# Performance work log

Hardware: AMD Instinct MI355X
Metric: run time of the kernel (lower is better)

## Reference

```python
import jax, jax.numpy as jnp
import numpy as np

# Dims
B_, L_, IN_ = 16, 8192, 57
DM, DS, HD, EXP, NL, OUT = 64, 32, 32, 2, 2, 6
DI = EXP * DM            # 128 inner dim
NH = DI // HD            # 4 heads
DPROJ = 2 * DI + 2 * DS + NH  # z, x, B, C, dt


def setup_inputs() -> dict:
    key = jax.random.key(0)
    ks = jax.random.split(key, 8)
    def rn(k, shape, scale=0.02):
        return jax.random.normal(k, shape, dtype=jnp.float32) * scale
    return {
        "x": jax.random.normal(ks[0], (B_, L_, IN_), dtype=jnp.float32),
        "W_in": rn(ks[1], (IN_, DM)),
        "b_in": jnp.zeros((DM,), jnp.float32),
        "in_proj_W": rn(ks[2], (NL, DM, DPROJ)),
        "in_proj_b": jnp.zeros((NL, DPROJ), jnp.float32),
        "A_log": jnp.log(jnp.broadcast_to(jnp.arange(1, NH + 1, dtype=jnp.float32), (NL, NH))),
        "D": jnp.ones((NL, NH), jnp.float32),
        "dt_bias": rn(ks[3], (NL, NH), 0.1),
        "out_proj_W": rn(ks[4], (NL, DI, DM)),
        "out_proj_b": jnp.zeros((NL, DM), jnp.float32),
        "cls_W": rn(ks[5], (DM, OUT)),
        "cls_b": jnp.zeros((OUT,), jnp.float32),
    }


def _mamba_layer(x, W, b, A_log, D, dt_bias, Wo, bo):
    """SISO Mamba3-style selective scan block. x: [B, L, DM]."""
    Bsz, L, _ = x.shape
    zxbcdt = x @ W + b                               # [B, L, DPROJ]
    z, xin, Bm, Cm, dt = jnp.split(
        zxbcdt, [DI, 2 * DI, 2 * DI + DS, 2 * DI + 2 * DS], axis=-1)
    dt = jax.nn.softplus(dt + dt_bias)               # [B, L, NH]
    A = -jnp.exp(A_log)                              # [NH], per-head scalar (SISO)
    xin = jax.nn.silu(xin).reshape(Bsz, L, NH, HD)   # [B, L, NH, HD]
    Bm = jax.nn.silu(Bm)                             # [B, L, DS]
    Cm = jax.nn.silu(Cm)                             # [B, L, DS]
    decay = jnp.exp(dt * A)                          # [B, L, NH]

    def step(h, inp):
        # h: [B, NH, HD, DS]
        xt, bt, ct, dtt, dect = inp
        h = dect[:, :, None, None] * h + (dtt[:, :, None] * xt)[..., None] * bt[:, None, None, :]
        yt = jnp.einsum('bhpn,bn->bhp', h, ct)       # [B, NH, HD]
        return h, yt

    h0 = jnp.zeros((Bsz, NH, HD, DS), x.dtype)
    xs = (jnp.moveaxis(xin, 1, 0), jnp.moveaxis(Bm, 1, 0), jnp.moveaxis(Cm, 1, 0),
          jnp.moveaxis(dt, 1, 0), jnp.moveaxis(decay, 1, 0))
    _, ys = jax.lax.scan(step, h0, xs)               # [L, B, NH, HD]
    y = jnp.moveaxis(ys, 0, 1) + D[None, None, :, None] * xin
    y = y.reshape(Bsz, L, DI) * jax.nn.silu(z)       # gated output
    return y @ Wo + bo                               # [B, L, DM]


def reference(x, W_in, b_in, in_proj_W, in_proj_b, A_log, D, dt_bias,
              out_proj_W, out_proj_b, cls_W, cls_b):
    h = x @ W_in + b_in                              # linear_in
    for l in range(NL):                              # residual Mamba stack
        h = h + _mamba_layer(h, in_proj_W[l], in_proj_b[l], A_log[l], D[l],
                             dt_bias[l], out_proj_W[l], out_proj_b[l])
    pooled = h.mean(axis=1)                          # AdaptiveAvgPool1d(1)
    return pooled @ cls_W + cls_b                    # classifier [B, OUT]
```

## Files before the change

### kernel.cpp

```cpp
#include <hip/hip_runtime.h>

#define BSZ   16
#define LSEQ  8192
#define DMDL  64
#define DSD   32
#define HDD   32
#define NHD   4
#define DIN   128
#define NLAY  2
#define NOUTC 6
#define DPRJ  324
#define QC    64
#define NCH   128
#define NT21  21

typedef __attribute__((ext_vector_type(8))) short bf16x8;
typedef __attribute__((ext_vector_type(4))) float f32x4;

__device__ float          g_h0[BSZ*LSEQ*DMDL];
__device__ unsigned short g_xy[BSZ*LSEQ*DIN];
__device__ unsigned short g_Ca[BSZ*LSEQ*DSD];
__device__ float          g_pc[BSZ*LSEQ*NHD];
__device__ float          g_cS[BSZ*NCH*NHD*HDD*DSD];
__device__ unsigned short g_Hb[BSZ*NCH*NHD*HDD*DSD];
__device__ float          g_cL[BSZ*NCH*NHD];
__device__ float          g_ppc[BSZ*NCH*DMDL];
__device__ unsigned short g_wf[NLAY*NT21*2*64*8];
__device__ unsigned short g_wo[NLAY*4*4*64*8];

__device__ __forceinline__ float silu_f(float v){ return v / (1.0f + __expf(-v)); }
__device__ __forceinline__ float softplus_f(float v){ return (v > 15.0f) ? v : __logf(1.0f + __expf(v)); }
__device__ __forceinline__ unsigned short f2bf(float f){
  union { float f; unsigned u; } v; v.f = f;
  unsigned r = v.u + 0x7FFFu + ((v.u >> 16) & 1u);
  return (unsigned short)(r >> 16);
}
__device__ __forceinline__ float bf2f(unsigned short h){
  union { unsigned u; float f; } v; v.u = ((unsigned)h) << 16;
  return v.f;
}

#define LSTR 132
__global__ __launch_bounds__(256) void k_linin(
    const float* __restrict__ x, const float* __restrict__ W,
    const float* __restrict__ bias)
{
  __shared__ float xt[57*LSTR];
  __shared__ float wl[57*64];
  const int tid = threadIdx.x;
  const long tb = (long)blockIdx.x * 128;
  for (int i = tid; i < 912; i += 256)
    *(float4*)&wl[i*4] = *(const float4*)&W[i*4];
  for (int i = tid; i < 1824; i += 256){
    float4 v = *(const float4*)&x[tb*57 + (long)i*4];
    const int e = i*4;
    int t0 = e / 57;
    int k0 = e - t0*57;
    float vv[4] = {v.x, v.y, v.z, v.w};
    #pragma unroll
    for (int j = 0; j < 4; ++j){
      int t = t0, k = k0 + j;
      if (k >= 57){ t += 1; k -= 57; }
      xt[k*LSTR + t] = vv[j];
    }
  }
  __syncthreads();
  const int d0 = (tid & 7) * 8;
  const int t0 = (tid >> 3) * 4;
  float acc[4][8];
  #pragma unroll
  for (int i = 0; i < 4; ++i)
    #pragma unroll
    for (int j = 0; j < 8; ++j) acc[i][j] = 0.f;
  #pragma unroll 4
  for (int k = 0; k < 57; ++k){
    float4 xv4 = *(const float4*)&xt[k*LSTR + t0];
    float4 w0  = *(const float4*)&wl[k*64 + d0];
    float4 w1  = *(const float4*)&wl[k*64 + d0 + 4];
    float xv[4] = {xv4.x, xv4.y, xv4.z, xv4.w};
    float wv[8] = {w0.x, w0.y, w0.z, w0.w, w1.x, w1.y, w1.z, w1.w};
    #pragma unroll
    for (int i = 0; i < 4; ++i)
      #pragma unroll
      for (int j = 0; j < 8; ++j) acc[i][j] += xv[i] * wv[j];
  }
  float4 bb0 = *(const float4*)&bias[d0];
  float4 bb1 = *(const float4*)&bias[d0 + 4];
  #pragma unroll
  for (int i = 0; i < 4; ++i){
    float4 o0, o1;
    o0.x = acc[i][0] + bb0.x; o0.y = acc[i][1] + bb0.y;
    o0.z = acc[i][2] + bb0.z; o0.w = acc[i][3] + bb0.w;
    o1.x = acc[i][4] + bb1.x; o1.y = acc[i][5] + bb1.y;
    o1.z = acc[i][6] + bb1.z; o1.w = acc[i][7] + bb1.w;
    *(float4*)&g_h0[(tb + t0 + i)*64 + d0]     = o0;
    *(float4*)&g_h0[(tb + t0 + i)*64 + d0 + 4] = o1;
  }
}

__global__ __launch_bounds__(128) void k_wprep(const float* __restrict__ W)
{
  const int nt = blockIdx.x;
  const int l  = blockIdx.y;
  const int ks = threadIdx.x >> 6, lane = threadIdx.x & 63;
  const float* Wl = W + (long)l*64*DPRJ;
  const int n  = nt*16 + (lane & 15);
  const int k0 = ks*32 + (lane >> 4)*8;
  unsigned short v[8];
  #pragma unroll
  for (int j = 0; j < 8; ++j)
    v[j] = (n < DPRJ) ? f2bf(Wl[(k0 + j)*DPRJ + n]) : (unsigned short)0;
  unsigned short* d = &g_wf[((((long)l*NT21 + nt)*2 + ks)*64 + lane)*8];
  *(ushort4*)&d[0] = make_ushort4(v[0], v[1], v[2], v[3]);
  *(ushort4*)&d[4] = make_ushort4(v[4], v[5], v[6], v[7]);
}

__global__ __launch_bounds__(64) void k_wprep2(const float* __restrict__ Wo)
{
  const int nt = blockIdx.x >> 2, ks = blockIdx.x & 3, l = blockIdx.y;
  const int lane = threadIdx.x;
  const int n  = nt*16 + (lane & 15);
  const int k0 = ks*32 + (lane >> 4)*8;
  const float* Wl = Wo + (long)l*128*64;
  unsigned short* d = &g_wo[((((long)l*4 + nt)*4 + ks)*64 + lane)*8];
  unsigned short v[8];
  #pragma unroll
  for (int j = 0; j < 8; ++j) v[j] = f2bf(Wl[(k0 + j)*64 + n]);
  *(ushort4*)&d[0] = make_ushort4(v[0], v[1], v[2], v[3]);
  *(ushort4*)&d[4] = make_ushort4(v[4], v[5], v[6], v[7]);
}

#define SB 40
#define ST 72
__device__ __forceinline__ int xsw(int p, int s){
  return p*ST + (((((s) >> 3) + ((p) >> 2)) & 7) << 3) + ((s) & 7);
}
__device__ __forceinline__ int xsw8(int p, int blk){
  return p*ST + (((((blk)) + ((p) >> 2)) & 7) << 3);
}
__global__ __launch_bounds__(256) void k_ps(
    const float* __restrict__ ipb, const float* __restrict__ dtb,
    const float* __restrict__ A_log, const float* __restrict__ Dp, int l)
{
  __shared__ __align__(16) unsigned short Afr[4*2*64*8];
  __shared__ __align__(16) unsigned short Bb[64*SB];
  __shared__ __align__(16) unsigned short Cb[64*SB];
  __shared__ __align__(16) unsigned short Bbt[32*ST];
  __shared__ __align__(16) unsigned short Xt[32*ST];
  __shared__ __align__(16) unsigned short Mb[64*ST];
  __shared__ float Sl[4*64];
  __shared__ float dts[4*64];
  __shared__ float wls[4*64];
  __shared__ float dtl[64*4];
  const int tid = threadIdx.x;
  const int cI = blockIdx.x, b = blockIdx.y;
  const long tb = (long)b*LSEQ + (long)cI*QC;
  for (int i = tid; i < 512; i += 256){
    const int t = i >> 3, k8 = i & 7;
    float4 f0 = *(const float4*)&g_h0[(tb + t)*64 + k8*8];
    float4 f1 = *(const float4*)&g_h0[(tb + t)*64 + k8*8 + 4];
    const int mt = t >> 4, ks = k8 >> 2, q = k8 & 3, ln = (t & 15) + 16*q;
    unsigned short* d = &Afr[(((mt*2 + ks)*64) + ln)*8];
    *(ushort4*)&d[0] = make_ushort4(f2bf(f0.x), f2bf(f0.y), f2bf(f0.z), f2bf(f0.w));
    *(ushort4*)&d[4] = make_ushort4(f2bf(f1.x), f2bf(f1.y), f2bf(f1.z), f2bf(f1.w));
  }
  __syncthreads();
  const int w = tid >> 6, lane = tid & 63;
  const int colq = lane & 15, rowq = lane >> 4;
  const float* bl = ipb + (long)l*DPRJ;
  const unsigned short* wf = &g_wf[(long)l*NT21*2*64*8];
  const bf16x8 a0 = *(const bf16x8*)&Afr[((w*2 + 0)*64 + lane)*8];
  const bf16x8 a1 = *(const bf16x8*)&Afr[((w*2 + 1)*64 + lane)*8];
  #pragma unroll
  for (int nti = 0; nti < 4; ++nti){
    const int nt = 16 + nti;
    bf16x8 b0 = *(const bf16x8*)&wf[((nt*2 + 0)*64 + lane)*8];
    bf16x8 b1 = *(const bf16x8*)&wf[((nt*2 + 1)*64 + lane)*8];
    const float bia = bl[nt*16 + colq];
    f32x4 acc = {0.f, 0.f, 0.f, 0.f};
    acc = __builtin_amdgcn_mfma_f32_16x16x32_bf16(a0, b0, acc, 0, 0, 0);
    acc = __builtin_amdgcn_mfma_f32_16x16x32_bf16(a1, b1, acc, 0, 0, 0);
    const int t4 = w*16 + rowq*4;
    if (nti < 2){
      const int n = nti*16 + colq;
      #pragma unroll
      for (int r = 0; r < 4; ++r){
        const unsigned short v = f2bf(silu_f(acc[r] + bia));
        Bb[(t4 + r)*SB + n] = v;
        Bbt[xsw(n, t4 + r)] = v;
      }
    } else {
      const int n = (nti - 2)*16 + colq;
      #pragma unroll
      for (int r = 0; r < 4; ++r)
        Cb[(t4 + r)*SB + n] = f2bf(silu_f(acc[r] + bia));
    }
  }
  {
    bf16x8 b0 = *(const bf16x8*)&wf[((20*2 + 0)*64 + lane)*8];
    bf16x8 b1 = *(const bf16x8*)&wf[((20*2 + 1)*64 + lane)*8];
    f32x4 acc = {0.f, 0.f, 0.f, 0.f};
    acc = __builtin_amdgcn_mfma_f32_16x16x32_bf16(a0, b0, acc, 0, 0, 0);
    acc = __builtin_amdgcn_mfma_f32_16x16x32_bf16(a1, b1, acc, 0, 0, 0);
    if (colq < 4){
      const float bia = bl[320 + colq] + dtb[l*4 + colq];
      const int t4 = w*16 + rowq*4;
      #pragma unroll
      for (int r = 0; r < 4; ++r)
        dtl[(t4 + r)*4 + colq] = softplus_f(acc[r] + bia);
    }
  }
  __syncthreads();
  {
    const int h = w, t = lane;
    const float Ah = -__expf(A_log[l*4 + h]);
    const float v = dtl[t*4 + h];
    float x = v * Ah;
    #pragma unroll
    for (int d = 1; d < 64; d <<= 1){
      float y = __shfl_up(x, d);
      if (t >= d) x += y;
    }
    Sl[h*64 + t] = x;
    dts[h*64 + t] = v;
    const float send = __shfl(x, 63);
    wls[h*64 + t] = __expf(send - x) * v;
    if (t == 63) g_cL[((long)b*NCH + cI)*4 + h] = x;
    g_pc[(tb + t)*4 + h] = __expf(x);
  }
  {
    const int t = tid >> 2, c0 = (tid & 3) * 8;
    *(uint4*)&g_Ca[(tb + t)*32 + c0] = *(const uint4*)&Cb[t*SB + c0];
  }
  float Greg[3][4];
  int Gmt[3], Gst[3];
  #pragma unroll
  for (int rep = 0; rep < 3; ++rep){
    const int k = w + rep*4;
    if (k < 10){
      const int mt = (k >= 6) ? 3 : ((k >= 3) ? 2 : ((k >= 1) ? 1 : 0));
      const int st = k - mt*(mt+1)/2;
      Gmt[rep] = mt; Gst[rep] = st;
      bf16x8 af = *(const bf16x8*)&Cb[(mt*16 + colq)*SB + rowq*8];
      bf16x8 bf = *(const bf16x8*)&Bb[(st*16 + colq)*SB + rowq*8];
      f32x4 acc = {0.f, 0.f, 0.f, 0.f};
      acc = __builtin_amdgcn_mfma_f32_16x16x32_bf16(af, bf, acc, 0, 0, 0);
      #pragma unroll
      for (int r = 0; r < 4; ++r) Greg[rep][r] = acc[r];
    } else { Gmt[rep] = -1; Gst[rep] = 0; }
  }
  #pragma unroll
  for (int rep = 0; rep < 2; ++rep){
    const int k = w + rep*4;
    if (k < 6){
      const int mt = (k < 3) ? 0 : ((k < 5) ? 1 : 2);
      const int st = (k < 3) ? (k + 1) : ((k < 5) ? (k - 1) : 3);
      #pragma unroll
      for (int r = 0; r < 4; ++r){
        const int t = mt*16 + rowq*4 + r, s = st*16 + colq;
        Mb[xsw(t, s)] = 0;
      }
    }
  }
  __syncthreads();
  for (int h = 0; h < NHD; ++h){
    #pragma unroll
    for (int half = 0; half < 2; ++half){
      const int nt = 8 + 2*h + half;
      bf16x8 b0 = *(const bf16x8*)&wf[((nt*2 + 0)*64 + lane)*8];
      bf16x8 b1 = *(const bf16x8*)&wf[((nt*2 + 1)*64 + lane)*8];
      const float bia = bl[nt*16 + colq];
      f32x4 acc = {0.f, 0.f, 0.f, 0.f};
      acc = __builtin_amdgcn_mfma_f32_16x16x32_bf16(a0, b0, acc, 0, 0, 0);
      acc = __builtin_amdgcn_mfma_f32_16x16x32_bf16(a1, b1, acc, 0, 0, 0);
      const int p = half*16 + colq;
      const int t4 = w*16 + rowq*4;
      #pragma unroll
      for (int r = 0; r < 4; ++r)
        Xt[xsw(p, t4 + r)] = f2bf(silu_f(acc[r] + bia));
    }
    #pragma unroll
    for (int rep = 0; rep < 3; ++rep){
      if (Gmt[rep] >= 0){
        const int mt = Gmt[rep], st = Gst[rep];
        const int s = st*16 + colq;
        const float sls = Sl[h*64 + s];
        const float dv = dts[h*64 + s];
        #pragma unroll
        for (int r = 0; r < 4; ++r){
          const int t = mt*16 + rowq*4 + r;
          const float m = (s <= t) ? __expf(Sl[h*64 + t] - sls) * dv * Greg[rep][r] : 0.f;
          Mb[xsw(t, s)] = f2bf(m);
        }
      }
    }
    __syncthreads();
    const float Dh = Dp[l*4 + h];
    bf16x8 ma0 = *(const bf16x8*)&Mb[xsw8(w*16 + colq, rowq)];
    bf16x8 ma1 = *(const bf16x8*)&Mb[xsw8(w*16 + colq, rowq + 4)];
    bf16x8 xb0, xb1;
    #pragma unroll
    for (int nt = 0; nt < 2; ++nt){
      bf16x8 b0 = *(const bf16x8*)&Xt[xsw8(nt*16 + colq, rowq)];
      bf16x8 b1 = *(const bf16x8*)&Xt[xsw8(nt*16 + colq, rowq + 4)];
      if (nt == (w & 1)){ xb0 = b0; xb1 = b1; }
      f32x4 acc = {0.f, 0.f, 0.f, 0.f};
      acc = __builtin_amdgcn_mfma_f32_16x16x32_bf16(ma0, b0, acc, 0, 0, 0);
      acc = __builtin_amdgcn_mfma_f32_16x16x32_bf16(ma1, b1, acc, 0, 0, 0);
      const int p = nt*16 + colq;
      #pragma unroll
      for (int r = 0; r < 4; ++r){
        const int t = w*16 + rowq*4 + r;
        const float xv = bf2f(Xt[xsw(p, t)]);
        g_xy[(tb + t)*128 + h*32 + p] = f2bf(acc[r] + Dh*xv);
      }
    }
    {
      union { bf16x8 v; unsigned short u[8]; } sx0, sx1, sa0, sa1;
      sx0.v = xb0; sx1.v = xb1;
      #pragma unroll
      for (int j = 0; j < 8; ++j){
        sa0.u[j] = f2bf(bf2f(sx0.u[j]) * wls[h*64 + rowq*8 + j]);
        sa1.u[j] = f2bf(bf2f(sx1.u[j]) * wls[h*64 + 32 + rowq*8 + j]);
      }
      const int mt = w & 1, nt2 = w >> 1;
      bf16x8 bb0 = *(const bf16x8*)&Bbt[xsw8(nt2*16 + colq, rowq)];
      bf16x8 bb1 = *(const bf16x8*)&Bbt[xsw8(nt2*16 + colq, rowq + 4)];
      f32x4 acc = {0.f, 0.f, 0.f, 0.f};
      acc = __builtin_amdgcn_mfma_f32_16x16x32_bf16(sa0.v, bb0, acc, 0, 0, 0);
      acc = __builtin_amdgcn_mfma_f32_16x16x32_bf16(sa1.v, bb1, acc, 0, 0, 0);
      const long base = (((long)b*NCH + cI)*NHD + h)*(HDD*DSD);
      const int n = nt2*16 + colq;
      #pragma unroll
      for (int r = 0; r < 4; ++r){
        const int p = mt*16 + rowq*4 + r;
        g_cS[base + p*32 + n] = acc[r];
      }
    }
    __syncthreads();
  }
}

__global__ __launch_bounds__(128) void k_s2()
{
  const int h = blockIdx.x >> 3, seg = blockIdx.x & 7, b = blockIdx.y;
  const int idx = seg*128 + threadIdx.x;
  float H = 0.f;
  for (int c = 0; c < NCH; ++c){
    const long o = (((long)b*NCH + c)*NHD + h)*1024 + idx;
    const float cs = g_cS[o];
    const float lg = g_cL[((long)b*NCH + c)*4 + h];
    g_Hb[o] = f2bf(H);
    H = __expf(lg) * H + cs;
  }
}

__global__ __launch_bounds__(256) void k_s3(
    const float* __restrict__ ipb, const float* __restrict__ bo, int l, int finalLayer)
{
  __shared__ __align__(16) unsigned short Hb[128*40];
  __shared__ __align__(16) unsigned short Cb[64*40];
  __shared__ __align__(16) unsigned short gl[64*136];
  __shared__ float pcl[4*64];
  __shared__ float csum[4*64];
  const int tid = threadIdx.x;
  const int cI = blockIdx.x, b = blockIdx.y;
  const long tb = (long)b*LSEQ + (long)cI*QC;
  const long hbase = (((long)b*NCH + cI)*NHD)*(long)(HDD*DSD);
  for (int i = tid; i < 512; i += 256){
    const int hp = i >> 2, n0 = (i & 3) * 8;
    *(uint4*)&Hb[hp*40 + n0] = *(const uint4*)&g_Hb[hbase + hp*32 + n0];
  }
  for (int i = tid; i < 512; i += 256){
    const int t = i >> 3, n0 = (i & 7) * 4;
    *(ushort4*)&Cb[t*40 + n0] = *(const ushort4*)&g_Ca[(tb + t)*32 + n0];
  }
  { int t = tid >> 2, h = tid & 3; pcl[h*64 + t] = g_pc[(tb + t)*4 + h]; }
  __syncthreads();
  const int w = tid >> 6, lane = tid & 63;
  const int colq = lane & 15, rowq = lane >> 4;
  const float* blz = ipb + (long)l*DPRJ;
  const unsigned short* wfz = &g_wf[(long)l*NT21*2*64*8];
  {
    const long tok0 = tb + w*16 + colq;
    bf16x8 h0a, h0b;
    {
      float4 f0 = *(const float4*)&g_h0[tok0*64 + rowq*8];
      float4 f1 = *(const float4*)&g_h0[tok0*64 + rowq*8 + 4];
      float4 f2 = *(const float4*)&g_h0[tok0*64 + 32 + rowq*8];
      float4 f3 = *(const float4*)&g_h0[tok0*64 + 32 + rowq*8 + 4];
      union { bf16x8 v; unsigned short u[8]; } ca, cb2;
      ca.u[0]=f2bf(f0.x); ca.u[1]=f2bf(f0.y); ca.u[2]=f2bf(f0.z); ca.u[3]=f2bf(f0.w);
      ca.u[4]=f2bf(f1.x); ca.u[5]=f2bf(f1.y); ca.u[6]=f2bf(f1.z); ca.u[7]=f2bf(f1.w);
      cb2.u[0]=f2bf(f2.x); cb2.u[1]=f2bf(f2.y); cb2.u[2]=f2bf(f2.z); cb2.u[3]=f2bf(f2.w);
      cb2.u[4]=f2bf(f3.x); cb2.u[5]=f2bf(f3.y); cb2.u[6]=f2bf(f3.z); cb2.u[7]=f2bf(f3.w);
      h0a = ca.v; h0b = cb2.v;
    }
    bf16x8 a = *(const bf16x8*)&Cb[(w*16 + colq)*40 + rowq*8];
    #pragma unroll
    for (int nt = 0; nt < 8; ++nt){
      bf16x8 bfr = *(const bf16x8*)&Hb[(nt*16 + colq)*40 + rowq*8];
      f32x4 acc = {0.f, 0.f, 0.f, 0.f};
      acc = __builtin_amdgcn_mfma_f32_16x16x32_bf16(a, bfr, acc, 0, 0, 0);
      bf16x8 bz0 = *(const bf16x8*)&wfz[((nt*2 + 0)*64 + lane)*8];
      bf16x8 bz1 = *(const bf16x8*)&wfz[((nt*2 + 1)*64 + lane)*8];
      f32x4 zac = {0.f, 0.f, 0.f, 0.f};
      zac = __builtin_amdgcn_mfma_f32_16x16x32_bf16(h0a, bz0, zac, 0, 0, 0);
      zac = __builtin_amdgcn_mfma_f32_16x16x32_bf16(h0b, bz1, zac, 0, 0, 0);
      const int hp = nt*16 + colq;
      const int h = hp >> 5;
      const float zb = blz[hp];
      #pragma unroll
      for (int r = 0; r < 4; ++r){
        const int t = w*16 + rowq*4 + r;
        const long tok = tb + t;
        const float v = pcl[h*64 + t] * acc[r] + bf2f(g_xy[tok*128 + hp]);
        gl[t*136 + hp] = f2bf(v * silu_f(zac[r] + zb));
      }
    }
  }
  __syncthreads();
  const unsigned short* wo = &g_wo[(long)l*4*4*512];
  #pragma unroll
  for (int nt2 = 0; nt2 < 4; ++nt2){
    f32x4 acc = {0.f, 0.f, 0.f, 0.f};
    #pragma unroll
    for (int ks = 0; ks < 4; ++ks){
      bf16x8 a = *(const bf16x8*)&gl[(w*16 + colq)*136 + ks*32 + rowq*8];
      bf16x8 bfr = *(const bf16x8*)&wo[(nt2*4 + ks)*512 + lane*8];
      acc = __builtin_amdgcn_mfma_f32_16x16x32_bf16(a, bfr, acc, 0, 0, 0);
    }
    const int dm = nt2*16 + colq;
    const float bb = bo[l*64 + dm];
    float part = 0.f;
    #pragma unroll
    for (int r = 0; r < 4; ++r){
      const int t = w*16 + rowq*4 + r;
      const long tok = tb + t;
      const float o = acc[r] + bb + g_h0[tok*64 + dm];
      g_h0[tok*64 + dm] = o;
      part += o;
    }
    if (finalLayer){
      part += __shfl_xor(part, 16);
      part += __shfl_xor(part, 32);
      if (rowq == 0) csum[w*64 + dm] = part;
    }
  }
  if (finalLayer){
    __syncthreads();
    if (tid < 64){
      g_ppc[((long)b*NCH + cI)*64 + tid] =
        csum[tid] + csum[64 + tid] + csum[128 + tid] + csum[192 + tid];
    }
  }
}

__global__ __launch_bounds__(64) void k_pool2(
    const float* __restrict__ cW, const float* __restrict__ cb,
    float* __restrict__ out)
{
  __shared__ float pl[64];
  const int b = blockIdx.x, tid = threadIdx.x;
  float s = 0.f;
  for (int c = 0; c < NCH; ++c) s += g_ppc[((long)b*NCH + c)*64 + tid];
  pl[tid] = s * (1.0f / 8192.0f);
  __syncthreads();
  if (tid < NOUTC){
    float acc = cb[tid];
    for (int dm = 0; dm < 64; ++dm) acc += pl[dm] * cW[dm*NOUTC + tid];
    out[b*NOUTC + tid] = acc;
  }
}

extern "C" void kernel_launch(void* const* d_in, const int* in_sizes, int n_in,
                              void* d_out, int out_size, void* d_ws, size_t ws_size,
                              hipStream_t stream)
{
  const float* x      = (const float*)d_in[0];
  const float* W_in   = (const float*)d_in[1];
  const float* b_in   = (const float*)d_in[2];
  const float* ipW    = (const float*)d_in[3];
  const float* ipb    = (const float*)d_in[4];
  const float* A_log  = (const float*)d_in[5];
  const float* Dp     = (const float*)d_in[6];
  const float* dtb    = (const float*)d_in[7];
  const float* opW    = (const float*)d_in[8];
  const float* opb    = (const float*)d_in[9];
  const float* clsW   = (const float*)d_in[10];
  const float* clsb   = (const float*)d_in[11];
  float* out = (float*)d_out;
  (void)d_ws; (void)ws_size;

  k_wprep<<<dim3(NT21, NLAY), 128, 0, stream>>>(ipW);
  k_wprep2<<<dim3(16, NLAY), 64, 0, stream>>>(opW);
  k_linin<<<1024, 256, 0, stream>>>(x, W_in, b_in);
  for (int l = 0; l < NLAY; ++l){
    k_ps<<<dim3(NCH, BSZ), 256, 0, stream>>>(ipb, dtb, A_log, Dp, l);
    k_s2<<<dim3(32, BSZ), 128, 0, stream>>>();
    k_s3<<<dim3(NCH, BSZ), 256, 0, stream>>>(ipb, opb, l, (l == NLAY-1) ? 1 : 0);
  }
  k_pool2<<<BSZ, 64, 0, stream>>>(clsW, clsb, out);
}
```

Before: 319.9 us.

## Use packed bf16 conversion, store chunk states in bf16, double-buffer per-head LDS

Swaps the manual float-to-bf16 rounding for the hardware packed convert instruction and widens the LDS stores. The chunk-state buffer g_cS moves from fp32 to bf16, halving its write and read traffic between k_ps and k_s2. The per-head Xt and Mb scratch buffers are double-buffered (Xt reuses the A-fragment buffer) so the trailing barrier in the head loop can be dropped. k_s2's chunk loop is also unrolled. The risk is lower precision in the inter-chunk state accumulation, plus possible hazards if the double-buffer reuse of the A-fragment region is unsafe.

```diff
diff --git a/kernel.cpp b/kernel.cpp
--- a/kernel.cpp
+++ b/kernel.cpp
@@ -21,7 +21,7 @@
 __device__ unsigned short g_xy[BSZ*LSEQ*DIN];
 __device__ unsigned short g_Ca[BSZ*LSEQ*DSD];
 __device__ float          g_pc[BSZ*LSEQ*NHD];
-__device__ float          g_cS[BSZ*NCH*NHD*HDD*DSD];
+__device__ unsigned short g_cS[BSZ*NCH*NHD*HDD*DSD];
 __device__ unsigned short g_Hb[BSZ*NCH*NHD*HDD*DSD];
 __device__ float          g_cL[BSZ*NCH*NHD];
 __device__ float          g_ppc[BSZ*NCH*DMDL];
@@ -38,6 +38,11 @@
 __device__ __forceinline__ float bf2f(unsigned short h){
   union { unsigned u; float f; } v; v.u = ((unsigned)h) << 16;
   return v.f;
+}
+__device__ __forceinline__ unsigned cvtpk(float lo, float hi){
+  unsigned r;
+  asm("v_cvt_pk_bf16_f32 %0, %1, %2" : "=v"(r) : "v"(lo), "v"(hi));
+  return r;
 }
 
 #define LSTR 132
@@ -142,12 +147,12 @@
     const float* __restrict__ ipb, const float* __restrict__ dtb,
     const float* __restrict__ A_log, const float* __restrict__ Dp, int l)
 {
-  __shared__ __align__(16) unsigned short Afr[4*2*64*8];
+  __shared__ __align__(16) unsigned short AfrX[4096];
   __shared__ __align__(16) unsigned short Bb[64*SB];
   __shared__ __align__(16) unsigned short Cb[64*SB];
   __shared__ __align__(16) unsigned short Bbt[32*ST];
-  __shared__ __align__(16) unsigned short Xt[32*ST];
-  __shared__ __align__(16) unsigned short Mb[64*ST];
+  __shared__ __align__(16) unsigned short Xt0[32*ST];
+  __shared__ __align__(16) unsigned short Mb[2*64*ST];
   __shared__ float Sl[4*64];
   __shared__ float dts[4*64];
   __shared__ float wls[4*64];
@@ -160,17 +165,19 @@
     float4 f0 = *(const float4*)&g_h0[(tb + t)*64 + k8*8];
     float4 f1 = *(const float4*)&g_h0[(tb + t)*64 + k8*8 + 4];
     const int mt = t >> 4, ks = k8 >> 2, q = k8 & 3, ln = (t & 15) + 16*q;
-    unsigned short* d = &Afr[(((mt*2 + ks)*64) + ln)*8];
-    *(ushort4*)&d[0] = make_ushort4(f2bf(f0.x), f2bf(f0.y), f2bf(f0.z), f2bf(f0.w));
-    *(ushort4*)&d[4] = make_ushort4(f2bf(f1.x), f2bf(f1.y), f2bf(f1.z), f2bf(f1.w));
+    uint4 pk;
+    pk.x = cvtpk(f0.x, f0.y); pk.y = cvtpk(f0.z, f0.w);
+    pk.z = cvtpk(f1.x, f1.y); pk.w = cvtpk(f1.z, f1.w);
+    *(uint4*)&AfrX[(((mt*2 + ks)*64) + ln)*8] = pk;
   }
   __syncthreads();
   const int w = tid >> 6, lane = tid & 63;
   const int colq = lane & 15, rowq = lane >> 4;
+  const int t4 = w*16 + rowq*4;
   const float* bl = ipb + (long)l*DPRJ;
   const unsigned short* wf = &g_wf[(long)l*NT21*2*64*8];
-  const bf16x8 a0 = *(const bf16x8*)&Afr[((w*2 + 0)*64 + lane)*8];
-  const bf16x8 a1 = *(const bf16x8*)&Afr[((w*2 + 1)*64 + lane)*8];
+  const bf16x8 a0 = *(const bf16x8*)&AfrX[((w*2 + 0)*64 + lane)*8];
+  const bf16x8 a1 = *(const bf16x8*)&AfrX[((w*2 + 1)*64 + lane)*8];
   #pragma unroll
   for (int nti = 0; nti < 4; ++nti){
     const int nt = 16 + nti;
@@ -180,20 +187,22 @@
     f32x4 acc = {0.f, 0.f, 0.f, 0.f};
     acc = __builtin_amdgcn_mfma_f32_16x16x32_bf16(a0, b0, acc, 0, 0, 0);
     acc = __builtin_amdgcn_mfma_f32_16x16x32_bf16(a1, b1, acc, 0, 0, 0);
-    const int t4 = w*16 + rowq*4;
+    const unsigned u0 = cvtpk(silu_f(acc[0] + bia), silu_f(acc[1] + bia));
+    const unsigned u1 = cvtpk(silu_f(acc[2] + bia), silu_f(acc[3] + bia));
     if (nti < 2){
       const int n = nti*16 + colq;
-      #pragma unroll
-      for (int r = 0; r < 4; ++r){
-        const unsigned short v = f2bf(silu_f(acc[r] + bia));
-        Bb[(t4 + r)*SB + n] = v;
-        Bbt[xsw(n, t4 + r)] = v;
-      }
+      uint2 uu; uu.x = u0; uu.y = u1;
+      *(uint2*)&Bbt[xsw(n, t4)] = uu;
+      Bb[(t4 + 0)*SB + n] = (unsigned short)(u0 & 0xFFFFu);
+      Bb[(t4 + 1)*SB + n] = (unsigned short)(u0 >> 16);
+      Bb[(t4 + 2)*SB + n] = (unsigned short)(u1 & 0xFFFFu);
+      Bb[(t4 + 3)*SB + n] = (unsigned short)(u1 >> 16);
     } else {
       const int n = (nti - 2)*16 + colq;
-      #pragma unroll
-      for (int r = 0; r < 4; ++r)
-        Cb[(t4 + r)*SB + n] = f2bf(silu_f(acc[r] + bia));
+      Cb[(t4 + 0)*SB + n] = (unsigned short)(u0 & 0xFFFFu);
+      Cb[(t4 + 1)*SB + n] = (unsigned short)(u0 >> 16);
+      Cb[(t4 + 2)*SB + n] = (unsigned short)(u1 & 0xFFFFu);
+      Cb[(t4 + 3)*SB + n] = (unsigned short)(u1 >> 16);
     }
   }
   {
@@ -204,7 +213,6 @@
     acc = __builtin_amdgcn_mfma_f32_16x16x32_bf16(a1, b1, acc, 0, 0, 0);
     if (colq < 4){
       const float bia = bl[320 + colq] + dtb[l*4 + colq];
-      const int t4 = w*16 + rowq*4;
       #pragma unroll
       for (int r = 0; r < 4; ++r)
         dtl[(t4 + r)*4 + colq] = softplus_f(acc[r] + bia);
@@ -259,11 +267,14 @@
       for (int r = 0; r < 4; ++r){
         const int t = mt*16 + rowq*4 + r, s = st*16 + colq;
         Mb[xsw(t, s)] = 0;
+        Mb[64*ST + xsw(t, s)] = 0;
       }
     }
   }
   __syncthreads();
   for (int h = 0; h < NHD; ++h){
+    unsigned short* Xt  = (h & 1) ? AfrX : Xt0;
+    unsigned short* Mbh = Mb + (h & 1)*64*ST;
     #pragma unroll
     for (int half = 0; half < 2; ++half){
       const int nt = 8 + 2*h + half;
@@ -273,11 +284,10 @@
       f32x4 acc = {0.f, 0.f, 0.f, 0.f};
       acc = __builtin_amdgcn_mfma_f32_16x16x32_bf16(a0, b0, acc, 0, 0, 0);
       acc = __builtin_amdgcn_mfma_f32_16x16x32_bf16(a1, b1, acc, 0, 0, 0);
-      const int p = half*16 + colq;
-      const int t4 = w*16 + rowq*4;
-      #pragma unroll
-      for (int r = 0; r < 4; ++r)
-        Xt[xsw(p, t4 + r)] = f2bf(silu_f(acc[r] + bia));
+      uint2 uu;
+      uu.x = cvtpk(silu_f(acc[0] + bia), silu_f(acc[1] + bia));
+      uu.y = cvtpk(silu_f(acc[2] + bia), silu_f(acc[3] + bia));
+      *(uint2*)&Xt[xsw(half*16 + colq, t4)] = uu;
     }
     #pragma unroll
     for (int rep = 0; rep < 3; ++rep){
@@ -290,14 +300,14 @@
         for (int r = 0; r < 4; ++r){
           const int t = mt*16 + rowq*4 + r;
           const float m = (s <= t) ? __expf(Sl[h*64 + t] - sls) * dv * Greg[rep][r] : 0.f;
-          Mb[xsw(t, s)] = f2bf(m);
+          Mbh[xsw(t, s)] = f2bf(m);
         }
       }
     }
     __syncthreads();
     const float Dh = Dp[l*4 + h];
-    bf16x8 ma0 = *(const bf16x8*)&Mb[xsw8(w*16 + colq, rowq)];
-    bf16x8 ma1 = *(const bf16x8*)&Mb[xsw8(w*16 + colq, rowq + 4)];
+    bf16x8 ma0 = *(const bf16x8*)&Mbh[xsw8(w*16 + colq, rowq)];
+    bf16x8 ma1 = *(const bf16x8*)&Mbh[xsw8(w*16 + colq, rowq + 4)];
     bf16x8 xb0, xb1;
     #pragma unroll
     for (int nt = 0; nt < 2; ++nt){
@@ -316,12 +326,15 @@
       }
     }
     {
-      union { bf16x8 v; unsigned short u[8]; } sx0, sx1, sa0, sa1;
+      union { bf16x8 v; unsigned short us[8]; } sx0, sx1;
+      union { bf16x8 v; unsigned u[4]; } sa0, sa1;
       sx0.v = xb0; sx1.v = xb1;
       #pragma unroll
-      for (int j = 0; j < 8; ++j){
-        sa0.u[j] = f2bf(bf2f(sx0.u[j]) * wls[h*64 + rowq*8 + j]);
-        sa1.u[j] = f2bf(bf2f(sx1.u[j]) * wls[h*64 + 32 + rowq*8 + j]);
+      for (int jj = 0; jj < 4; ++jj){
+        sa0.u[jj] = cvtpk(bf2f(sx0.us[2*jj])   * wls[h*64 + rowq*8 + 2*jj],
+                          bf2f(sx0.us[2*jj+1]) * wls[h*64 + rowq*8 + 2*jj + 1]);
+        sa1.u[jj] = cvtpk(bf2f(sx1.us[2*jj])   * wls[h*64 + 32 + rowq*8 + 2*jj],
+                          bf2f(sx1.us[2*jj+1]) * wls[h*64 + 32 + rowq*8 + 2*jj + 1]);
       }
       const int mt = w & 1, nt2 = w >> 1;
       bf16x8 bb0 = *(const bf16x8*)&Bbt[xsw8(nt2*16 + colq, rowq)];
@@ -334,10 +347,9 @@
       #pragma unroll
       for (int r = 0; r < 4; ++r){
         const int p = mt*16 + rowq*4 + r;
-        g_cS[base + p*32 + n] = acc[r];
+        g_cS[base + p*32 + n] = f2bf(acc[r]);
       }
     }
-    __syncthreads();
   }
 }
 
@@ -346,9 +358,10 @@
   const int h = blockIdx.x >> 3, seg = blockIdx.x & 7, b = blockIdx.y;
   const int idx = seg*128 + threadIdx.x;
   float H = 0.f;
+  #pragma unroll 4
   for (int c = 0; c < NCH; ++c){
     const long o = (((long)b*NCH + c)*NHD + h)*1024 + idx;
-    const float cs = g_cS[o];
+    const float cs = bf2f(g_cS[o]);
     const float lg = g_cL[((long)b*NCH + c)*4 + h];
     g_Hb[o] = f2bf(H);
     H = __expf(lg) * H + cs;
@@ -389,11 +402,11 @@
       float4 f1 = *(const float4*)&g_h0[tok0*64 + rowq*8 + 4];
       float4 f2 = *(const float4*)&g_h0[tok0*64 + 32 + rowq*8];
       float4 f3 = *(const float4*)&g_h0[tok0*64 + 32 + rowq*8 + 4];
-      union { bf16x8 v; unsigned short u[8]; } ca, cb2;
-      ca.u[0]=f2bf(f0.x); ca.u[1]=f2bf(f0.y); ca.u[2]=f2bf(f0.z); ca.u[3]=f2bf(f0.w);
-      ca.u[4]=f2bf(f1.x); ca.u[5]=f2bf(f1.y); ca.u[6]=f2bf(f1.z); ca.u[7]=f2bf(f1.w);
-      cb2.u[0]=f2bf(f2.x); cb2.u[1]=f2bf(f2.y); cb2.u[2]=f2bf(f2.z); cb2.u[3]=f2bf(f2.w);
-      cb2.u[4]=f2bf(f3.x); cb2.u[5]=f2bf(f3.y); cb2.u[6]=f2bf(f3.z); cb2.u[7]=f2bf(f3.w);
+      union { bf16x8 v; unsigned u[4]; } ca, cb2;
+      ca.u[0] = cvtpk(f0.x, f0.y); ca.u[1] = cvtpk(f0.z, f0.w);
+      ca.u[2] = cvtpk(f1.x, f1.y); ca.u[3] = cvtpk(f1.z, f1.w);
+      cb2.u[0] = cvtpk(f2.x, f2.y); cb2.u[1] = cvtpk(f2.z, f2.w);
+      cb2.u[2] = cvtpk(f3.x, f3.y); cb2.u[3] = cvtpk(f3.z, f3.w);
       h0a = ca.v; h0b = cb2.v;
     }
     bf16x8 a = *(const bf16x8*)&Cb[(w*16 + colq)*40 + rowq*8];
```

Result: faster. 310.8 us (-2.8%).
